# Kernel tuning notes

Measured on AMD Instinct MI355X. Metric: run time of the kernel, lower is better.

## Reference

```python
import jax, jax.numpy as jnp
import numpy as np

N, E, D, H = 100000, 600000, 128, 8
C = D // H  # head dim = 16


def layer_norm(x, g, b, eps=1e-5):
    mu = jnp.mean(x, axis=-1, keepdims=True)
    var = jnp.mean(jnp.square(x - mu), axis=-1, keepdims=True)
    return (x - mu) * jax.lax.rsqrt(var + eps) * g + b


def setup_inputs() -> dict:
    key = jax.random.key(0)
    ks = jax.random.split(key, 20)
    s = 1.0 / np.sqrt(D)
    u = lambda k, shp: jax.random.uniform(k, shp, jnp.float32, -s, s)
    return {
        "edge_index": jax.random.randint(ks[0], (2, E), 0, N, dtype=jnp.int64),
        "node_attr": jax.random.normal(ks[1], (N, D), jnp.float32),
        "edge_attr": jax.random.normal(ks[2], (E, D), jnp.float32),
        # TransformerConv params (PyG: lin_query/key/value with bias, lin_edge no bias, lin_skip with bias)
        "Wq": u(ks[3], (D, D)), "bq": u(ks[4], (D,)),
        "Wk": u(ks[5], (D, D)), "bk": u(ks[6], (D,)),
        "Wv": u(ks[7], (D, D)), "bv": u(ks[8], (D,)),
        "We": u(ks[9], (D, D)),
        "Wskip": u(ks[10], (D, D)), "bskip": u(ks[11], (D,)),
        # FFN
        "W1": u(ks[12], (D, D)), "b1": u(ks[13], (D,)),
        "W2": u(ks[14], (D, D)), "b2": u(ks[15], (D,)),
        # LayerNorms
        "g1": jnp.ones((D,)), "be1": jnp.zeros((D,)),
        "g2": jnp.ones((D,)), "be2": jnp.zeros((D,)),
    }


def reference(edge_index, node_attr, edge_attr, Wq, bq, Wk, bk, Wv, bv, We,
              Wskip, bskip, W1, b1, W2, b2, g1, be1, g2, be2):
    src, dst = edge_index[0], edge_index[1]  # j -> i (source_to_target)
    x = node_attr
    q = (x @ Wq + bq).reshape(N, H, C)
    k = (x @ Wk + bk).reshape(N, H, C)
    v = (x @ Wv + bv).reshape(N, H, C)
    e = (edge_attr @ We).reshape(E, H, C)

    ke = k[src] + e                               # [E,H,C]
    alpha = jnp.sum(q[dst] * ke, axis=-1) / np.sqrt(C)  # [E,H]
    # scatter-softmax over edges grouped by destination node
    amax = jax.ops.segment_max(alpha, dst, num_segments=N)
    ex = jnp.exp(alpha - amax[dst])
    denom = jax.ops.segment_sum(ex, dst, num_segments=N)
    alpha = ex / (denom[dst] + 1e-16)             # [E,H]  (dropout=0 at eval)

    msg = alpha[..., None] * (v[src] + e)         # [E,H,C]
    out = jax.ops.segment_sum(msg, dst, num_segments=N).reshape(N, D)
    out = out + x @ Wskip + bskip                 # root_weight skip

    h = x + layer_norm(out, g1, be1)
    ffn = jax.nn.silu(h @ W1 + b1) @ W2 + b2
    return h + layer_norm(ffn, g2, be2)
```

## Files before the change

### kernel.cpp

```cpp
#include <hip/hip_runtime.h>
#include <hip/hip_bf16.h>

typedef __attribute__((ext_vector_type(8))) short short8;
typedef __attribute__((ext_vector_type(4))) short short4v;
typedef __attribute__((ext_vector_type(4))) float floatx4;

#define D128 128

__device__ __forceinline__ short f2bf(float f) {
    union { float f; unsigned u; } x; x.f = f;
    unsigned r = x.u + 0x7FFFu + ((x.u >> 16) & 1u);
    return (short)(r >> 16);
}
__device__ __forceinline__ float bflo(unsigned u) { return __uint_as_float(u << 16); }
__device__ __forceinline__ float bfhi(unsigned u) { return __uint_as_float(u & 0xffff0000u); }

__global__ void wprep_kernel(const float* Wq, const float* Wk, const float* Wv,
                             const float* We, const float* Ws, const float* W1,
                             const float* W2, short* wt) {
    const float* src;
    switch (blockIdx.x) {
        case 0: src = Wq; break;
        case 1: src = Wk; break;
        case 2: src = Wv; break;
        case 3: src = Ws; break;
        case 4: src = We; break;
        case 5: src = W1; break;
        default: src = W2; break;
    }
    short* dst = wt + (size_t)blockIdx.x * D128 * D128;
    for (int i = threadIdx.x; i < D128 * D128; i += blockDim.x) {
        int k = i >> 7, n = i & 127;
        dst[n * D128 + k] = f2bf(src[i]);
    }
}

__device__ __forceinline__ void load_W(const short* __restrict__ Wt, short* Bs) {
    const short8* wp = (const short8*)Wt;
    const int tid = threadIdx.x;
#pragma unroll
    for (int it = 0; it < 8; ++it) {
        int i = it * 256 + tid;
        int n = i >> 4, kg = i & 15;
        *(short8*)(&Bs[n * 136 + kg * 8]) = wp[i];
    }
    __syncthreads();
}

template <typename TA, typename TO, int SILU>
__device__ __forceinline__ void gemm_core(const TA* __restrict__ A,
                                          const float* __restrict__ bias,
                                          TO* __restrict__ out, int M,
                                          const short* Bs,
                                          const int* __restrict__ rowmap) {
    const int tid = threadIdx.x;
    const int wv = tid >> 6, lane = tid & 63;
    const int m = lane & 15, quad = lane >> 4;
    const int ntiles = (M + 63) >> 6;

    for (int tile = blockIdx.x; tile < ntiles; tile += gridDim.x) {
        const int row = tile * 64 + wv * 16 + m;
        const bool valid = row < M;

        short8 af[4];
        if constexpr (sizeof(TA) == 4) {
            const float* ap = (const float*)A + (size_t)row * D128;
#pragma unroll
            for (int kk = 0; kk < 4; ++kk) {
                float4 u0 = make_float4(0.f, 0.f, 0.f, 0.f), u1 = u0;
                if (valid) {
                    u0 = *(const float4*)(ap + kk * 32 + quad * 8);
                    u1 = *(const float4*)(ap + kk * 32 + quad * 8 + 4);
                }
                short8 s;
                s[0] = f2bf(u0.x); s[1] = f2bf(u0.y); s[2] = f2bf(u0.z); s[3] = f2bf(u0.w);
                s[4] = f2bf(u1.x); s[5] = f2bf(u1.y); s[6] = f2bf(u1.z); s[7] = f2bf(u1.w);
                af[kk] = s;
            }
        } else {
            const short8* ap = (const short8*)((const short*)A + (size_t)row * D128);
#pragma unroll
            for (int kk = 0; kk < 4; ++kk) {
                short8 s;
#pragma unroll
                for (int j = 0; j < 8; ++j) s[j] = 0;
                if (valid) s = ap[kk * 4 + quad];
                af[kk] = s;
            }
        }

        floatx4 acc[8];
#pragma unroll
        for (int t = 0; t < 8; ++t) acc[t] = (floatx4){0.f, 0.f, 0.f, 0.f};

#pragma unroll
        for (int kk = 0; kk < 4; ++kk) {
            const int kq = kk * 32 + quad * 8;
#pragma unroll
            for (int t = 0; t < 8; ++t) {
                short8 bf = *(const short8*)(&Bs[(t * 16 + m) * 136 + kq]);
                acc[t] = __builtin_amdgcn_mfma_f32_16x16x32_bf16(bf, af[kk], acc[t], 0, 0, 0);
            }
        }

        if (valid) {
            size_t orow = rowmap ? (size_t)rowmap[row] : (size_t)row;
            TO* op = out + orow * D128;
#pragma unroll
            for (int t = 0; t < 8; ++t) {
                const int c = t * 16 + quad * 4;
                floatx4 bv = (floatx4){0.f, 0.f, 0.f, 0.f};
                if (bias) bv = *(const floatx4*)(bias + c);
                float v0 = acc[t][0] + bv[0];
                float v1 = acc[t][1] + bv[1];
                float v2 = acc[t][2] + bv[2];
                float v3 = acc[t][3] + bv[3];
                if (SILU) {
                    v0 = v0 / (1.f + __expf(-v0));
                    v1 = v1 / (1.f + __expf(-v1));
                    v2 = v2 / (1.f + __expf(-v2));
                    v3 = v3 / (1.f + __expf(-v3));
                }
                if constexpr (sizeof(TO) == 4) {
                    *(floatx4*)(op + c) = (floatx4){v0, v1, v2, v3};
                } else {
                    short4v s;
                    s.x = f2bf(v0); s.y = f2bf(v1); s.z = f2bf(v2); s.w = f2bf(v3);
                    *(short4v*)(op + c) = s;
                }
            }
        }
    }
}

template <typename TA, typename TO, int SILU>
__global__ __launch_bounds__(256) void gemmP(const TA* __restrict__ A,
                                             const short* __restrict__ Wt,
                                             const float* __restrict__ bias,
                                             TO* __restrict__ out, int M,
                                             const int* __restrict__ rowmap) {
    __shared__ __attribute__((aligned(16))) short Bs[128 * 136];
    load_W(Wt, Bs);
    gemm_core<TA, TO, SILU>(A, bias, out, M, Bs, rowmap);
}

__global__ __launch_bounds__(256) void gemm_qkvs(const float* __restrict__ x,
                                                 const short* __restrict__ wt,
                                                 const float* __restrict__ bq,
                                                 const float* __restrict__ bk,
                                                 const float* __restrict__ bv,
                                                 const float* __restrict__ bs,
                                                 short* __restrict__ q,
                                                 short* __restrict__ k,
                                                 short* __restrict__ v,
                                                 short* __restrict__ s, int M) {
    __shared__ __attribute__((aligned(16))) short Bs[128 * 136];
    const int y = blockIdx.y;
    load_W(wt + (size_t)y * 16384, Bs);
    const float* bias = (y == 0) ? bq : (y == 1) ? bk : (y == 2) ? bv : bs;
    short* out = (y == 0) ? q : (y == 1) ? k : (y == 2) ? v : s;
    gemm_core<float, short, 0>(x, bias, out, M, Bs, nullptr);
}

__global__ __launch_bounds__(256) void gemm_ln_out(const short* __restrict__ A,
                                                   const short* __restrict__ Wt,
                                                   const float* __restrict__ bias,
                                                   const float* __restrict__ h,
                                                   const float* __restrict__ g,
                                                   const float* __restrict__ b,
                                                   float* __restrict__ out, int M) {
    __shared__ __attribute__((aligned(16))) short Bs[128 * 136];
    load_W(Wt, Bs);
    const int tid = threadIdx.x;
    const int wv = tid >> 6, lane = tid & 63;
    const int m = lane & 15, quad = lane >> 4;
    const int ntiles = (M + 63) >> 6;

    for (int tile = blockIdx.x; tile < ntiles; tile += gridDim.x) {
        const int row = tile * 64 + wv * 16 + m;
        const bool valid = row < M;

        short8 af[4];
        const short8* ap = (const short8*)(A + (size_t)row * D128);
#pragma unroll
        for (int kk = 0; kk < 4; ++kk) {
            short8 s;
#pragma unroll
            for (int j = 0; j < 8; ++j) s[j] = 0;
            if (valid) s = ap[kk * 4 + quad];
            af[kk] = s;
        }

        floatx4 acc[8];
#pragma unroll
        for (int t = 0; t < 8; ++t) acc[t] = (floatx4){0.f, 0.f, 0.f, 0.f};

#pragma unroll
        for (int kk = 0; kk < 4; ++kk) {
            const int kq = kk * 32 + quad * 8;
#pragma unroll
            for (int t = 0; t < 8; ++t) {
                short8 bf = *(const short8*)(&Bs[(t * 16 + m) * 136 + kq]);
                acc[t] = __builtin_amdgcn_mfma_f32_16x16x32_bf16(bf, af[kk], acc[t], 0, 0, 0);
            }
        }

        float vals[8][4];
        float sum = 0.f;
#pragma unroll
        for (int t = 0; t < 8; ++t) {
            const int c = t * 16 + quad * 4;
            floatx4 bv = *(const floatx4*)(bias + c);
#pragma unroll
            for (int r = 0; r < 4; ++r) {
                float v = acc[t][r] + bv[r];
                vals[t][r] = v;
                sum += v;
            }
        }
        sum += __shfl_xor(sum, 16);
        sum += __shfl_xor(sum, 32);
        float mu = sum * (1.f / 128.f);
        float vs = 0.f;
#pragma unroll
        for (int t = 0; t < 8; ++t)
#pragma unroll
            for (int r = 0; r < 4; ++r) {
                float d = vals[t][r] - mu;
                vals[t][r] = d;
                vs += d * d;
            }
        vs += __shfl_xor(vs, 16);
        vs += __shfl_xor(vs, 32);
        float rs = rsqrtf(vs * (1.f / 128.f) + 1e-5f);

        if (valid) {
            const float* hp = h + (size_t)row * D128;
            float* op = out + (size_t)row * D128;
#pragma unroll
            for (int t = 0; t < 8; ++t) {
                const int c = t * 16 + quad * 4;
                floatx4 hv = *(const floatx4*)(hp + c);
                floatx4 gv = *(const floatx4*)(g + c);
                floatx4 bb = *(const floatx4*)(b + c);
                floatx4 o;
#pragma unroll
                for (int r = 0; r < 4; ++r) o[r] = hv[r] + vals[t][r] * rs * gv[r] + bb[r];
                *(floatx4*)(op + c) = o;
            }
        }
    }
}

__global__ void hist_kernel(const int* __restrict__ ei, int* __restrict__ deg, int E) {
    int i = blockIdx.x * 256 + threadIdx.x;
    if (i < E) atomicAdd(&deg[ei[(size_t)E + i]], 1);
}

__global__ __launch_bounds__(256) void scan_a(const int* __restrict__ deg,
                                              int* __restrict__ rowstart,
                                              int* __restrict__ partials, int N) {
    __shared__ int lds[256];
    int base = blockIdx.x * 1024;
    int t = threadIdx.x;
    int v[4];
    int s = 0;
#pragma unroll
    for (int j = 0; j < 4; ++j) {
        int i = base + t * 4 + j;
        v[j] = (i < N) ? deg[i] : 0;
        s += v[j];
    }
    lds[t] = s;
    __syncthreads();
    int val = s;
    for (int off = 1; off < 256; off <<= 1) {
        int other = (t >= off) ? lds[t - off] : 0;
        __syncthreads();
        val += other;
        lds[t] = val;
        __syncthreads();
    }
    int excl = val - s;
#pragma unroll
    for (int j = 0; j < 4; ++j) {
        int i = base + t * 4 + j;
        if (i < N) rowstart[i] = excl;
        excl += v[j];
    }
    if (t == 255) partials[blockIdx.x] = val;
}

__global__ __launch_bounds__(256) void scan_b(int* __restrict__ partials, int n) {
    __shared__ int lds[256];
    int t = threadIdx.x;
    int s = (t < n) ? partials[t] : 0;
    lds[t] = s;
    __syncthreads();
    int val = s;
    for (int off = 1; off < 256; off <<= 1) {
        int other = (t >= off) ? lds[t - off] : 0;
        __syncthreads();
        val += other;
        lds[t] = val;
        __syncthreads();
    }
    if (t < n) partials[t] = val - s;
}

__global__ void scan_c(int* __restrict__ rowstart, const int* __restrict__ partials,
                       int* __restrict__ cursor, int N, int Etot) {
    int i = blockIdx.x * 256 + threadIdx.x;
    if (i < N) {
        int v = rowstart[i] + partials[i >> 10];
        rowstart[i] = v;
        cursor[i] = v;
    }
    if (i == 0) rowstart[N] = Etot;
}

__global__ void fill_kernel(const int* __restrict__ ei, int* __restrict__ cursor,
                            int* __restrict__ csrc, int* __restrict__ pos, int E) {
    int i = blockIdx.x * 256 + threadIdx.x;
    if (i >= E) return;
    int src = ei[i], dst = ei[(size_t)E + i];
    int slot = atomicAdd(&cursor[dst], 1);
    csrc[slot] = src;
    pos[i] = slot;
}

__global__ __launch_bounds__(256) void attn_ln_h(const int* __restrict__ rowstart,
                                                 const int* __restrict__ csrc,
                                                 const unsigned* __restrict__ q2,
                                                 const unsigned* __restrict__ k2,
                                                 const unsigned* __restrict__ v2,
                                                 const unsigned* __restrict__ ep2,
                                                 const unsigned* __restrict__ skip2,
                                                 const float* __restrict__ x,
                                                 const float* __restrict__ g,
                                                 const float* __restrict__ b,
                                                 float* __restrict__ h, int N) {
    int t = threadIdx.x;
    int node = blockIdx.x * 4 + (t >> 6);
    if (node >= N) return;
    int l = t & 63;
    unsigned qu = q2[(size_t)node * 64 + l];
    float q0 = bflo(qu), q1 = bfhi(qu);
    int p0 = rowstart[node], p1 = rowstart[node + 1];
    float num0 = 0.f, num1 = 0.f, den = 0.f;
    int p = p0;
    for (; p + 1 < p1; p += 2) {
        int s0 = csrc[p], s1 = csrc[p + 1];
        unsigned ku0 = k2[(size_t)s0 * 64 + l];
        unsigned ku1 = k2[(size_t)s1 * 64 + l];
        unsigned eu0 = ep2[(size_t)p * 64 + l];
        unsigned eu1 = ep2[(size_t)(p + 1) * 64 + l];
        unsigned vu0 = v2[(size_t)s0 * 64 + l];
        unsigned vu1 = v2[(size_t)s1 * 64 + l];
        float ka0 = bflo(ku0) + bflo(eu0), kb0 = bfhi(ku0) + bfhi(eu0);
        float pd0 = q0 * ka0 + q1 * kb0;
        float ka1 = bflo(ku1) + bflo(eu1), kb1 = bfhi(ku1) + bfhi(eu1);
        float pd1 = q0 * ka1 + q1 * kb1;
        pd0 += __shfl_xor(pd0, 1); pd1 += __shfl_xor(pd1, 1);
        pd0 += __shfl_xor(pd0, 2); pd1 += __shfl_xor(pd1, 2);
        pd0 += __shfl_xor(pd0, 4); pd1 += __shfl_xor(pd1, 4);
        float ex0 = __expf(pd0 * 0.25f);
        float ex1 = __expf(pd1 * 0.25f);
        den += ex0 + ex1;
        num0 += ex0 * (bflo(vu0) + bflo(eu0)) + ex1 * (bflo(vu1) + bflo(eu1));
        num1 += ex0 * (bfhi(vu0) + bfhi(eu0)) + ex1 * (bfhi(vu1) + bfhi(eu1));
    }
    if (p < p1) {
        int s0 = csrc[p];
        unsigned ku = k2[(size_t)s0 * 64 + l];
        unsigned eu = ep2[(size_t)p * 64 + l];
        unsigned vu = v2[(size_t)s0 * 64 + l];
        float ka = bflo(ku) + bflo(eu), kb = bfhi(ku) + bfhi(eu);
        float pd = q0 * ka + q1 * kb;
        pd += __shfl_xor(pd, 1);
        pd += __shfl_xor(pd, 2);
        pd += __shfl_xor(pd, 4);
        float ex = __expf(pd * 0.25f);
        den += ex;
        num0 += ex * (bflo(vu) + bflo(eu));
        num1 += ex * (bfhi(vu) + bfhi(eu));
    }
    float inv = 1.f / (den + 1e-16f);
    float v0 = num0 * inv, v1 = num1 * inv;

    unsigned su = skip2[(size_t)node * 64 + l];
    v0 += bflo(su); v1 += bfhi(su);
    float sum = v0 + v1;
#pragma unroll
    for (int o = 32; o > 0; o >>= 1) sum += __shfl_xor(sum, o);
    float mu = sum * (1.f / 128.f);
    float d0 = v0 - mu, d1 = v1 - mu;
    float vs = d0 * d0 + d1 * d1;
#pragma unroll
    for (int o = 32; o > 0; o >>= 1) vs += __shfl_xor(vs, o);
    float rs = rsqrtf(vs * (1.f / 128.f) + 1e-5f);
    int c0 = l * 2;
    size_t base = (size_t)node * D128;
    float2 xe = *(const float2*)(x + base + c0);
    float2 o2;
    o2.x = xe.x + d0 * rs * g[c0] + b[c0];
    o2.y = xe.y + d1 * rs * g[c0 + 1] + b[c0 + 1];
    *(float2*)(h + base + c0) = o2;
}

extern "C" void kernel_launch(void* const* d_in, const int* in_sizes, int n_in,
                              void* d_out, int out_size, void* d_ws, size_t ws_size,
                              hipStream_t stream) {
    const int*   ei    = (const int*)d_in[0];
    const float* x     = (const float*)d_in[1];
    const float* ea    = (const float*)d_in[2];
    const float* Wq    = (const float*)d_in[3];
    const float* bq    = (const float*)d_in[4];
    const float* Wk    = (const float*)d_in[5];
    const float* bk    = (const float*)d_in[6];
    const float* Wv    = (const float*)d_in[7];
    const float* bv    = (const float*)d_in[8];
    const float* We    = (const float*)d_in[9];
    const float* Wsk   = (const float*)d_in[10];
    const float* bskip = (const float*)d_in[11];
    const float* W1    = (const float*)d_in[12];
    const float* b1    = (const float*)d_in[13];
    const float* W2    = (const float*)d_in[14];
    const float* b2    = (const float*)d_in[15];
    const float* g1    = (const float*)d_in[16];
    const float* be1   = (const float*)d_in[17];
    const float* g2    = (const float*)d_in[18];
    const float* be2   = (const float*)d_in[19];

    const int N = in_sizes[1] / D128;
    const int E = in_sizes[2] / D128;
    const size_t nd = (size_t)N * D128;
    const size_t ed = (size_t)E * D128;

    char* p = (char*)d_ws;
    auto alloc = [&](size_t bytes) {
        char* r = p;
        p += (bytes + 255) & ~(size_t)255;
        return (void*)r;
    };
    short* qb       = (short*)alloc(nd * 2);
    short* kb       = (short*)alloc(nd * 2);
    short* vb       = (short*)alloc(nd * 2);
    short* sb       = (short*)alloc(nd * 2);
    short* ebuf     = (short*)alloc(ed * 2);
    float* h        = (float*)alloc(nd * 4);
    short* t1b      = (short*)alloc(nd * 2);
    short* wt       = (short*)alloc(7 * 16384 * 2);
    int*   deg      = (int*)alloc((size_t)N * 4);
    int*   rowstart = (int*)alloc(((size_t)N + 1) * 4);
    int*   partials = (int*)alloc(512 * 4);
    int*   cursor   = (int*)alloc((size_t)N * 4);
    int*   csrc     = (int*)alloc((size_t)E * 4);
    int*   pos      = (int*)alloc((size_t)E * 4);

    const int tilesN = (N + 63) / 64;
    const int tilesE = (E + 63) / 64;
    const int gxN = tilesN < 1024 ? tilesN : 1024;
    const int gxE = tilesE < 1024 ? tilesE : 1024;
    const int gxQ = tilesN < 512 ? tilesN : 512;
    const int nchunks = (N + 1023) / 1024;

    wprep_kernel<<<7, 256, 0, stream>>>(Wq, Wk, Wv, We, Wsk, W1, W2, wt);

    hipMemsetAsync(deg, 0, (size_t)N * 4, stream);
    hist_kernel<<<(E + 255) / 256, 256, 0, stream>>>(ei, deg, E);
    scan_a<<<nchunks, 256, 0, stream>>>(deg, rowstart, partials, N);
    scan_b<<<1, 256, 0, stream>>>(partials, nchunks);
    scan_c<<<(N + 255) / 256, 256, 0, stream>>>(rowstart, partials, cursor, N, E);
    fill_kernel<<<(E + 255) / 256, 256, 0, stream>>>(ei, cursor, csrc, pos, E);

    gemm_qkvs<<<dim3(gxQ, 4), 256, 0, stream>>>(x, wt, bq, bk, bv, bskip,
                                                qb, kb, vb, sb, N);
    gemmP<float, short, 0><<<gxE, 256, 0, stream>>>(ea, wt + 4 * 16384, nullptr, ebuf, E, pos);

    attn_ln_h<<<(N + 3) / 4, 256, 0, stream>>>(rowstart, csrc, (const unsigned*)qb,
                                               (const unsigned*)kb, (const unsigned*)vb,
                                               (const unsigned*)ebuf, (const unsigned*)sb,
                                               x, g1, be1, h, N);

    gemmP<float, short, 1><<<gxN, 256, 0, stream>>>(h, wt + 5 * 16384, b1, t1b, N, nullptr);
    gemm_ln_out<<<gxN, 256, 0, stream>>>(t1b, wt + 6 * 16384, b2, h, g2, be2,
                                         (float*)d_out, N);
}
```

Before: 839.0 us.

## Fuse projection GEMMs into one launch, fuse FFN GEMMs, unroll attention by four

Merges the QKV/skip projection and the edge projection into a single heterogeneous launch, with block ranges split between edge and node work. Fuses the two FFN GEMMs into one kernel that keeps the SiLU intermediate in registers, moving it into MFMA operand layout with lane shuffles. This drops the bf16 intermediate buffer and one launch. The attention edge loop is unrolled from two to four edges for more memory-level parallelism. The costs are doubled LDS per FFN block, which may lower occupancy, and higher register pressure.

```diff
diff --git a/kernel.cpp b/kernel.cpp
--- a/kernel.cpp
+++ b/kernel.cpp
@@ -52,13 +52,14 @@
                                           const float* __restrict__ bias,
                                           TO* __restrict__ out, int M,
                                           const short* Bs,
-                                          const int* __restrict__ rowmap) {
+                                          const int* __restrict__ rowmap,
+                                          int b0, int bstep) {
     const int tid = threadIdx.x;
     const int wv = tid >> 6, lane = tid & 63;
     const int m = lane & 15, quad = lane >> 4;
     const int ntiles = (M + 63) >> 6;
 
-    for (int tile = blockIdx.x; tile < ntiles; tile += gridDim.x) {
+    for (int tile = b0; tile < ntiles; tile += bstep) {
         const int row = tile * 64 + wv * 16 + m;
         const bool valid = row < M;
 
@@ -133,75 +134,137 @@
     }
 }
 
-template <typename TA, typename TO, int SILU>
-__global__ __launch_bounds__(256) void gemmP(const TA* __restrict__ A,
-                                             const short* __restrict__ Wt,
-                                             const float* __restrict__ bias,
-                                             TO* __restrict__ out, int M,
-                                             const int* __restrict__ rowmap) {
+__global__ __launch_bounds__(256) void proj_all(const float* __restrict__ x,
+                                                const float* __restrict__ ea,
+                                                const short* __restrict__ wt,
+                                                const float* __restrict__ bq,
+                                                const float* __restrict__ bk,
+                                                const float* __restrict__ bvv,
+                                                const float* __restrict__ bs,
+                                                short* __restrict__ q,
+                                                short* __restrict__ k,
+                                                short* __restrict__ v,
+                                                short* __restrict__ s,
+                                                short* __restrict__ eb,
+                                                const int* __restrict__ pos,
+                                                int N, int E, int nbE, int nbQ) {
     __shared__ __attribute__((aligned(16))) short Bs[128 * 136];
-    load_W(Wt, Bs);
-    gemm_core<TA, TO, SILU>(A, bias, out, M, Bs, rowmap);
-}
-
-__global__ __launch_bounds__(256) void gemm_qkvs(const float* __restrict__ x,
-                                                 const short* __restrict__ wt,
-                                                 const float* __restrict__ bq,
-                                                 const float* __restrict__ bk,
-                                                 const float* __restrict__ bv,
-                                                 const float* __restrict__ bs,
-                                                 short* __restrict__ q,
-                                                 short* __restrict__ k,
-                                                 short* __restrict__ v,
-                                                 short* __restrict__ s, int M) {
-    __shared__ __attribute__((aligned(16))) short Bs[128 * 136];
-    const int y = blockIdx.y;
-    load_W(wt + (size_t)y * 16384, Bs);
-    const float* bias = (y == 0) ? bq : (y == 1) ? bk : (y == 2) ? bv : bs;
-    short* out = (y == 0) ? q : (y == 1) ? k : (y == 2) ? v : s;
-    gemm_core<float, short, 0>(x, bias, out, M, Bs, nullptr);
-}
-
-__global__ __launch_bounds__(256) void gemm_ln_out(const short* __restrict__ A,
-                                                   const short* __restrict__ Wt,
-                                                   const float* __restrict__ bias,
-                                                   const float* __restrict__ h,
-                                                   const float* __restrict__ g,
-                                                   const float* __restrict__ b,
-                                                   float* __restrict__ out, int M) {
-    __shared__ __attribute__((aligned(16))) short Bs[128 * 136];
-    load_W(Wt, Bs);
+    const int b = blockIdx.x;
+    if (b < nbE) {
+        load_W(wt + 4 * 16384, Bs);
+        gemm_core<float, short, 0>(ea, nullptr, eb, E, Bs, pos, b, nbE);
+    } else {
+        const int y = (b - nbE) / nbQ, b2 = (b - nbE) % nbQ;
+        load_W(wt + (size_t)y * 16384, Bs);
+        const float* bias = (y == 0) ? bq : (y == 1) ? bk : (y == 2) ? bvv : bs;
+        short* o = (y == 0) ? q : (y == 1) ? k : (y == 2) ? v : s;
+        gemm_core<float, short, 0>(x, bias, o, N, Bs, nullptr, b2, nbQ);
+    }
+}
+
+__global__ __launch_bounds__(256) void ffn_fused(const float* __restrict__ h,
+                                                 const short* __restrict__ Wt1,
+                                                 const short* __restrict__ Wt2,
+                                                 const float* __restrict__ b1,
+                                                 const float* __restrict__ b2,
+                                                 const float* __restrict__ g,
+                                                 const float* __restrict__ be,
+                                                 float* __restrict__ out, int M) {
+    __shared__ __attribute__((aligned(16))) short Bs1[128 * 136];
+    __shared__ __attribute__((aligned(16))) short Bs2[128 * 136];
+    {
+        const short8* wp1 = (const short8*)Wt1;
+        const short8* wp2 = (const short8*)Wt2;
+        const int tid = threadIdx.x;
+#pragma unroll
+        for (int it = 0; it < 8; ++it) {
+            int i = it * 256 + tid;
+            int n = i >> 4, kg = i & 15;
+            *(short8*)(&Bs1[n * 136 + kg * 8]) = wp1[i];
+            *(short8*)(&Bs2[n * 136 + kg * 8]) = wp2[i];
+        }
+        __syncthreads();
+    }
     const int tid = threadIdx.x;
     const int wv = tid >> 6, lane = tid & 63;
     const int m = lane & 15, quad = lane >> 4;
+    const int qh = quad >> 1;
+    const int srcA = ((quad & 1) << 5) + m;
     const int ntiles = (M + 63) >> 6;
 
     for (int tile = blockIdx.x; tile < ntiles; tile += gridDim.x) {
         const int row = tile * 64 + wv * 16 + m;
         const bool valid = row < M;
+        const float* hp = h + (size_t)row * D128;
 
         short8 af[4];
-        const short8* ap = (const short8*)(A + (size_t)row * D128);
 #pragma unroll
         for (int kk = 0; kk < 4; ++kk) {
-            short8 s;
-#pragma unroll
-            for (int j = 0; j < 8; ++j) s[j] = 0;
-            if (valid) s = ap[kk * 4 + quad];
-            af[kk] = s;
+            float4 u0v = make_float4(0.f, 0.f, 0.f, 0.f), u1v = u0v;
+            if (valid) {
+                u0v = *(const float4*)(hp + kk * 32 + quad * 8);
+                u1v = *(const float4*)(hp + kk * 32 + quad * 8 + 4);
+            }
+            short8 sfr;
+            sfr[0] = f2bf(u0v.x); sfr[1] = f2bf(u0v.y); sfr[2] = f2bf(u0v.z); sfr[3] = f2bf(u0v.w);
+            sfr[4] = f2bf(u1v.x); sfr[5] = f2bf(u1v.y); sfr[6] = f2bf(u1v.z); sfr[7] = f2bf(u1v.w);
+            af[kk] = sfr;
         }
 
         floatx4 acc[8];
 #pragma unroll
         for (int t = 0; t < 8; ++t) acc[t] = (floatx4){0.f, 0.f, 0.f, 0.f};
-
 #pragma unroll
         for (int kk = 0; kk < 4; ++kk) {
             const int kq = kk * 32 + quad * 8;
 #pragma unroll
             for (int t = 0; t < 8; ++t) {
-                short8 bf = *(const short8*)(&Bs[(t * 16 + m) * 136 + kq]);
+                short8 bf = *(const short8*)(&Bs1[(t * 16 + m) * 136 + kq]);
                 acc[t] = __builtin_amdgcn_mfma_f32_16x16x32_bf16(bf, af[kk], acc[t], 0, 0, 0);
+            }
+        }
+
+        unsigned u0[8], u1[8];
+#pragma unroll
+        for (int t = 0; t < 8; ++t) {
+            const int c = t * 16 + quad * 4;
+            floatx4 bv = *(const floatx4*)(b1 + c);
+            float w0 = acc[t][0] + bv[0], w1 = acc[t][1] + bv[1];
+            float w2 = acc[t][2] + bv[2], w3 = acc[t][3] + bv[3];
+            w0 = w0 / (1.f + __expf(-w0));
+            w1 = w1 / (1.f + __expf(-w1));
+            w2 = w2 / (1.f + __expf(-w2));
+            w3 = w3 / (1.f + __expf(-w3));
+            u0[t] = (unsigned)(unsigned short)f2bf(w0) | ((unsigned)(unsigned short)f2bf(w1) << 16);
+            u1[t] = (unsigned)(unsigned short)f2bf(w2) | ((unsigned)(unsigned short)f2bf(w3) << 16);
+        }
+
+        short8 af2[4];
+#pragma unroll
+        for (int kk = 0; kk < 4; ++kk) {
+            const int tA = 2 * kk, tB = 2 * kk + 1;
+            unsigned a0 = __shfl(u0[tA], srcA),      c0 = __shfl(u0[tB], srcA);
+            unsigned a1 = __shfl(u1[tA], srcA),      c1 = __shfl(u1[tB], srcA);
+            unsigned a2 = __shfl(u0[tA], srcA + 16), c2 = __shfl(u0[tB], srcA + 16);
+            unsigned a3 = __shfl(u1[tA], srcA + 16), c3 = __shfl(u1[tB], srcA + 16);
+            union { unsigned u[4]; short8 s; } cv;
+            cv.u[0] = qh ? c0 : a0;
+            cv.u[1] = qh ? c1 : a1;
+            cv.u[2] = qh ? c2 : a2;
+            cv.u[3] = qh ? c3 : a3;
+            af2[kk] = cv.s;
+        }
+
+        floatx4 acc2[8];
+#pragma unroll
+        for (int t = 0; t < 8; ++t) acc2[t] = (floatx4){0.f, 0.f, 0.f, 0.f};
+#pragma unroll
+        for (int kk = 0; kk < 4; ++kk) {
+            const int kq = kk * 32 + quad * 8;
+#pragma unroll
+            for (int t = 0; t < 8; ++t) {
+                short8 bf = *(const short8*)(&Bs2[(t * 16 + m) * 136 + kq]);
+                acc2[t] = __builtin_amdgcn_mfma_f32_16x16x32_bf16(bf, af2[kk], acc2[t], 0, 0, 0);
             }
         }
 
@@ -210,12 +273,12 @@
 #pragma unroll
         for (int t = 0; t < 8; ++t) {
             const int c = t * 16 + quad * 4;
-            floatx4 bv = *(const floatx4*)(bias + c);
+            floatx4 bv = *(const floatx4*)(b2 + c);
 #pragma unroll
             for (int r = 0; r < 4; ++r) {
-                float v = acc[t][r] + bv[r];
-                vals[t][r] = v;
-                sum += v;
+                float vv = acc2[t][r] + bv[r];
+                vals[t][r] = vv;
+                sum += vv;
             }
         }
         sum += __shfl_xor(sum, 16);
@@ -235,14 +298,13 @@
         float rs = rsqrtf(vs * (1.f / 128.f) + 1e-5f);
 
         if (valid) {
-            const float* hp = h + (size_t)row * D128;
             float* op = out + (size_t)row * D128;
 #pragma unroll
             for (int t = 0; t < 8; ++t) {
                 const int c = t * 16 + quad * 4;
                 floatx4 hv = *(const floatx4*)(hp + c);
                 floatx4 gv = *(const floatx4*)(g + c);
-                floatx4 bb = *(const floatx4*)(b + c);
+                floatx4 bb = *(const floatx4*)(be + c);
                 floatx4 o;
 #pragma unroll
                 for (int r = 0; r < 4; ++r) o[r] = hv[r] + vals[t][r] * rs * gv[r] + bb[r];
@@ -349,34 +411,46 @@
     int p0 = rowstart[node], p1 = rowstart[node + 1];
     float num0 = 0.f, num1 = 0.f, den = 0.f;
     int p = p0;
-    for (; p + 1 < p1; p += 2) {
-        int s0 = csrc[p], s1 = csrc[p + 1];
+    for (; p + 3 < p1; p += 4) {
+        int s0 = csrc[p], s1 = csrc[p + 1], s2 = csrc[p + 2], s3 = csrc[p + 3];
         unsigned ku0 = k2[(size_t)s0 * 64 + l];
         unsigned ku1 = k2[(size_t)s1 * 64 + l];
+        unsigned ku2 = k2[(size_t)s2 * 64 + l];
+        unsigned ku3 = k2[(size_t)s3 * 64 + l];
         unsigned eu0 = ep2[(size_t)p * 64 + l];
         unsigned eu1 = ep2[(size_t)(p + 1) * 64 + l];
+        unsigned eu2 = ep2[(size_t)(p + 2) * 64 + l];
+        unsigned eu3 = ep2[(size_t)(p + 3) * 64 + l];
         unsigned vu0 = v2[(size_t)s0 * 64 + l];
         unsigned vu1 = v2[(size_t)s1 * 64 + l];
-        float ka0 = bflo(ku0) + bflo(eu0), kb0 = bfhi(ku0) + bfhi(eu0);
-        float pd0 = q0 * ka0 + q1 * kb0;
-        float ka1 = bflo(ku1) + bflo(eu1), kb1 = bfhi(ku1) + bfhi(eu1);
-        float pd1 = q0 * ka1 + q1 * kb1;
+        unsigned vu2 = v2[(size_t)s2 * 64 + l];
+        unsigned vu3 = v2[(size_t)s3 * 64 + l];
+        float pd0 = q0 * (bflo(ku0) + bflo(eu0)) + q1 * (bfhi(ku0) + bfhi(eu0));
+        float pd1 = q0 * (bflo(ku1) + bflo(eu1)) + q1 * (bfhi(ku1) + bfhi(eu1));
+        float pd2 = q0 * (bflo(ku2) + bflo(eu2)) + q1 * (bfhi(ku2) + bfhi(eu2));
+        float pd3 = q0 * (bflo(ku3) + bflo(eu3)) + q1 * (bfhi(ku3) + bfhi(eu3));
         pd0 += __shfl_xor(pd0, 1); pd1 += __shfl_xor(pd1, 1);
+        pd2 += __shfl_xor(pd2, 1); pd3 += __shfl_xor(pd3, 1);
         pd0 += __shfl_xor(pd0, 2); pd1 += __shfl_xor(pd1, 2);
+        pd2 += __shfl_xor(pd2, 2); pd3 += __shfl_xor(pd3, 2);
         pd0 += __shfl_xor(pd0, 4); pd1 += __shfl_xor(pd1, 4);
+        pd2 += __shfl_xor(pd2, 4); pd3 += __shfl_xor(pd3, 4);
         float ex0 = __expf(pd0 * 0.25f);
         float ex1 = __expf(pd1 * 0.25f);
-        den += ex0 + ex1;
-        num0 += ex0 * (bflo(vu0) + bflo(eu0)) + ex1 * (bflo(vu1) + bflo(eu1));
-        num1 += ex0 * (bfhi(vu0) + bfhi(eu0)) + ex1 * (bfhi(vu1) + bfhi(eu1));
-    }
-    if (p < p1) {
+        float ex2 = __expf(pd2 * 0.25f);
+        float ex3 = __expf(pd3 * 0.25f);
+        den += (ex0 + ex1) + (ex2 + ex3);
+        num0 += ex0 * (bflo(vu0) + bflo(eu0)) + ex1 * (bflo(vu1) + bflo(eu1))
+              + ex2 * (bflo(vu2) + bflo(eu2)) + ex3 * (bflo(vu3) + bflo(eu3));
+        num1 += ex0 * (bfhi(vu0) + bfhi(eu0)) + ex1 * (bfhi(vu1) + bfhi(eu1))
+              + ex2 * (bfhi(vu2) + bfhi(eu2)) + ex3 * (bfhi(vu3) + bfhi(eu3));
+    }
+    for (; p < p1; ++p) {
         int s0 = csrc[p];
         unsigned ku = k2[(size_t)s0 * 64 + l];
         unsigned eu = ep2[(size_t)p * 64 + l];
         unsigned vu = v2[(size_t)s0 * 64 + l];
-        float ka = bflo(ku) + bflo(eu), kb = bfhi(ku) + bfhi(eu);
-        float pd = q0 * ka + q1 * kb;
+        float pd = q0 * (bflo(ku) + bflo(eu)) + q1 * (bfhi(ku) + bfhi(eu));
         pd += __shfl_xor(pd, 1);
         pd += __shfl_xor(pd, 2);
         pd += __shfl_xor(pd, 4);
@@ -449,7 +523,6 @@
     short* sb       = (short*)alloc(nd * 2);
     short* ebuf     = (short*)alloc(ed * 2);
     float* h        = (float*)alloc(nd * 4);
-    short* t1b      = (short*)alloc(nd * 2);
     short* wt       = (short*)alloc(7 * 16384 * 2);
     int*   deg      = (int*)alloc((size_t)N * 4);
     int*   rowstart = (int*)alloc(((size_t)N + 1) * 4);
@@ -460,9 +533,9 @@
 
     const int tilesN = (N + 63) / 64;
     const int tilesE = (E + 63) / 64;
-    const int gxN = tilesN < 1024 ? tilesN : 1024;
-    const int gxE = tilesE < 1024 ? tilesE : 1024;
-    const int gxQ = tilesN < 512 ? tilesN : 512;
+    const int nbE = tilesE < 1536 ? tilesE : 1536;
+    const int nbQ = tilesN < 256 ? tilesN : 256;
+    const int gxF = tilesN < 1024 ? tilesN : 1024;
     const int nchunks = (N + 1023) / 1024;
 
     wprep_kernel<<<7, 256, 0, stream>>>(Wq, Wk, Wv, We, Wsk, W1, W2, wt);
@@ -474,16 +547,15 @@
     scan_c<<<(N + 255) / 256, 256, 0, stream>>>(rowstart, partials, cursor, N, E);
     fill_kernel<<<(E + 255) / 256, 256, 0, stream>>>(ei, cursor, csrc, pos, E);
 
-    gemm_qkvs<<<dim3(gxQ, 4), 256, 0, stream>>>(x, wt, bq, bk, bv, bskip,
-                                                qb, kb, vb, sb, N);
-    gemmP<float, short, 0><<<gxE, 256, 0, stream>>>(ea, wt + 4 * 16384, nullptr, ebuf, E, pos);
+    proj_all<<<nbE + 4 * nbQ, 256, 0, stream>>>(x, ea, wt, bq, bk, bv, bskip,
+                                                qb, kb, vb, sb, ebuf, pos,
+                                                N, E, nbE, nbQ);
 
     attn_ln_h<<<(N + 3) / 4, 256, 0, stream>>>(rowstart, csrc, (const unsigned*)qb,
                                                (const unsigned*)kb, (const unsigned*)vb,
                                                (const unsigned*)ebuf, (const unsigned*)sb,
                                                x, g1, be1, h, N);
 
-    gemmP<float, short, 1><<<gxN, 256, 0, stream>>>(h, wt + 5 * 16384, b1, t1b, N, nullptr);
-    gemm_ln_out<<<gxN, 256, 0, stream>>>(t1b, wt + 6 * 16384, b2, h, g2, be2,
-                                         (float*)d_out, N);
-}
+    ffn_fused<<<gxF, 256, 0, stream>>>(h, wt + 5 * 16384, wt + 6 * 16384,
+                                       b1, b2, g2, be2, (float*)d_out, N);
+}
```

Result: faster. 804.0 us (-4.2%).
